# Optimization experiments

Measured on AMD Instinct MI355X. Metric: run time of the kernel, lower is better.

## Reference

```python
import jax, jax.numpy as jnp
import numpy as np

EPS = 1e-12


def setup_inputs() -> dict:
    key = jax.random.key(0)
    n, k, Eu, iterations = 200_000, 7, 1_600_000, 3
    k1, k2, k3 = jax.random.split(key, 3)
    # undirected edge list; each undirected edge yields two directed edges
    su = jax.random.randint(k1, (Eu,), 0, n, dtype=jnp.int32)
    du = jax.random.randint(k2, (Eu,), 0, n, dtype=jnp.int32)
    src = jnp.concatenate([su, du])                                   # [E]
    dst = jnp.concatenate([du, su])                                   # [E]
    rev = jnp.concatenate([jnp.arange(Eu, 2 * Eu, dtype=jnp.int32),
                           jnp.arange(Eu, dtype=jnp.int32)])          # [E]
    # node priors (rows sum to 1), mimicking the soft label priors
    prior = jax.random.uniform(k3, (n, k), minval=0.1, maxval=1.0)
    prior = prior / prior.sum(axis=1, keepdims=True)
    # label-to-label potential: log(beta) on the diagonal (beta = 3.0)
    W = jnp.log(3.0) * jnp.eye(k, dtype=jnp.float32)
    return {"prior": prior, "W": W, "src": src, "dst": dst,
            "rev": rev, "iterations": iterations}


def reference(prior, W, src, dst, rev, iterations):
    n, k = prior.shape
    E = src.shape[0]
    psi = jnp.exp(jnp.clip(W, -10.0, 10.0))                           # [k,k]
    msgs = jnp.full((E, k), 1.0 / k, dtype=prior.dtype)

    def step(msgs, _):
        # product of incoming messages per node, in log-space (msgs >= EPS)
        logm = jnp.log(msgs)                                          # [E,k]
        logP = jax.ops.segment_sum(logm, dst, num_segments=n)         # [n,k]
        # per directed edge (i -> j): remove reverse message j -> i
        prod_in_i = jnp.exp(logP[src] - logm[rev])                    # [E,k]
        b = jnp.maximum(prior[src] * prod_in_i, EPS)                  # [E,k]
        m_new = jnp.maximum(b @ psi, EPS)                             # [E,k]
        m_new = m_new / jnp.maximum(m_new.sum(-1, keepdims=True), EPS)
        return m_new, None

    msgs, _ = jax.lax.scan(step, msgs, None, length=int(iterations))

    # beliefs
    logP = jax.ops.segment_sum(jnp.log(msgs), dst, num_segments=n)    # [n,k]
    b = jnp.maximum(prior * jnp.exp(logP), EPS)
    return b / jnp.maximum(b.sum(-1, keepdims=True), EPS)
```

## Files before the change

### kernel.cpp

```cpp
#include <hip/hip_runtime.h>
#include <hip/hip_bf16.h>

#define K 7
#define EPSF 1e-12f
#define LOG_INV_K (-1.9459101090932196f)
#define LOG7 1.9459101090932196f
#define NEG_LOG_EPS 27.631021f
#define SBN 512
#define SBSH 9
#define NSBMAX 768
#define PB 256

#define QSB 409.59375f
#define QSO 2047.96875f
#define QIB (160.0f / 65535.0f)
#define QIO (32.0f / 65535.0f)

__device__ __forceinline__ float ldf(const void* p, size_t idx, int mode) {
    return mode ? ((const float*)p)[idx]
                : __bfloat162float(((const __hip_bfloat16*)p)[idx]);
}

__device__ __forceinline__ void load_psi(const void* W, float* psi, int mode) {
    if (threadIdx.x < K * K) {
        float w = ldf(W, threadIdx.x, mode);
        w = fminf(fmaxf(w, -10.f), 10.f);
        psi[threadIdx.x] = __expf(w);
    }
    __syncthreads();
}

__device__ __forceinline__ void bp_lin(const float* b, const float* psi, float* m) {
    float o[K], sum = 0.f;
#pragma unroll
    for (int j = 0; j < K; j++) {
        float acc = 0.f;
#pragma unroll
        for (int i = 0; i < K; i++) acc += b[i] * psi[i * K + j];
        o[j] = fmaxf(acc, EPSF);
        sum += o[j];
    }
    float inv = __fdividef(1.f, fmaxf(sum, EPSF));
#pragma unroll
    for (int j = 0; j < K; j++) m[j] = o[j] * inv;
}

__device__ __forceinline__ void acc_log_msg(const float* b, const float* psi, float* acc) {
    float m[K];
    bp_lin(b, psi, m);
#pragma unroll
    for (int j = 0; j < K; j++) acc[j] += __logf(m[j]);
}

__device__ __forceinline__ void ld8(const float* base, float* r) {
    const float4* p = (const float4*)base;
    float4 a = p[0], b = p[1];
    r[0]=a.x; r[1]=a.y; r[2]=a.z; r[3]=a.w; r[4]=b.x; r[5]=b.y; r[6]=b.z; r[7]=b.w;
}

__device__ __forceinline__ void dec_pd(uint4 w, float* p, int* degv, int* u1) {
    p[0] = __uint_as_float((w.x & 0xffffu) << 16);
    p[1] = __uint_as_float(w.x & 0xffff0000u);
    p[2] = __uint_as_float((w.y & 0xffffu) << 16);
    p[3] = __uint_as_float(w.y & 0xffff0000u);
    p[4] = __uint_as_float((w.z & 0xffffu) << 16);
    p[5] = __uint_as_float(w.z & 0xffff0000u);
    p[6] = __uint_as_float((w.w & 0xffffu) << 16);
    *degv = (int)((w.w >> 16) & 0x7fffu);
    *u1 = (int)(w.w >> 31);
}

__device__ __forceinline__ uint4 enc_log7(const float* le) {
    float mx = le[0];
#pragma unroll
    for (int i = 1; i < K; i++) mx = fmaxf(mx, le[i]);
    float nb = fminf(fmaxf(-mx, 0.f), 159.9f);
    unsigned qb = (unsigned)(nb * QSB + 0.5f);
    unsigned qo[K];
#pragma unroll
    for (int i = 0; i < K; i++)
        qo[i] = (unsigned)(fminf(mx - le[i], 31.98f) * QSO + 0.5f);
    uint4 r;
    r.x = qb | (qo[0] << 16);
    r.y = qo[1] | (qo[2] << 16);
    r.z = qo[3] | (qo[4] << 16);
    r.w = qo[5] | (qo[6] << 16);
    return r;
}

__device__ __forceinline__ void dec_exp7(uint4 w, float* e) {
    float base = (float)(w.x & 0xffffu) * QIB;
    float o[K];
    o[0] = (float)(w.x >> 16) * QIO;
    o[1] = (float)(w.y & 0xffffu) * QIO;
    o[2] = (float)(w.y >> 16) * QIO;
    o[3] = (float)(w.z & 0xffffu) * QIO;
    o[4] = (float)(w.z >> 16) * QIO;
    o[5] = (float)(w.w & 0xffffu) * QIO;
    o[6] = (float)(w.w >> 16) * QIO;
#pragma unroll
    for (int i = 0; i < K; i++) e[i] = __expf(-(base + o[i]));
}

__global__ void sniff8_kernel(const void* __restrict__ W, int* __restrict__ prm) {
    if (blockIdx.x != 0 || threadIdx.x != 0) return;
    const unsigned int* Wraw = (const unsigned int*)W;
    int mode = ((Wraw[0] >> 16) != 0u) ? 1 : 0;
    float diag0 = 0.f, offd0 = 0.f;
    int structured = 1;
    for (int i = 0; i < K; i++)
        for (int j = 0; j < K; j++) {
            float w = ldf(W, i * K + j, mode);
            w = fminf(fmaxf(w, -10.f), 10.f);
            float e = __expf(w);
            if (i == 0 && j == 0) diag0 = e;
            if (i == 0 && j == 1) offd0 = e;
            if (i == j) { if (i > 0 && e != diag0) structured = 0; }
            else       { if (!(i == 0 && j == 1) && e != offd0) structured = 0; }
        }
    if (!(offd0 >= 0.2f) || !(diag0 >= offd0)) structured = 0;
    prm[0] = mode | (structured << 1);
    ((float*)prm)[1] = offd0;
    ((float*)prm)[2] = diag0;
}

__global__ void hist6_kernel(const int* __restrict__ dst, int* __restrict__ hist,
                             int* __restrict__ btot, int E, int EPB, int NSB) {
    __shared__ int h[NSBMAX];
    for (int i = threadIdx.x; i < NSB; i += 256) h[i] = 0;
    __syncthreads();
    int blk = blockIdx.x;
    int e0 = blk * EPB, e1 = min(e0 + EPB, E);
    for (int e = e0 + (int)threadIdx.x; e < e1; e += 256)
        atomicAdd(&h[dst[e] >> SBSH], 1);
    __syncthreads();
    for (int i = threadIdx.x; i < NSB; i += 256) {
        int c = h[i];
        hist[i * PB + blk] = c;
        if (c) atomicAdd(&btot[i], c);
    }
}

__global__ void bscan6_kernel(const int* __restrict__ btot, int* __restrict__ boff, int NSB) {
    __shared__ int s[1024];
    int t = threadIdx.x;
    int x = (t < NSB) ? btot[t] : 0;
    s[t] = x;
    __syncthreads();
    for (int o = 1; o < 1024; o <<= 1) {
        int y = (t >= o) ? s[t - o] : 0;
        __syncthreads();
        s[t] += y;
        __syncthreads();
    }
    if (t < NSB) boff[t] = s[t] - x;
    if (t == NSB - 1) boff[NSB] = s[t];
}

__global__ void sscan6_kernel(const int* __restrict__ hist, const int* __restrict__ boff,
                              int* __restrict__ woff) {
    __shared__ int s[PB];
    int b = blockIdx.x, t = threadIdx.x;
    int x = hist[b * PB + t];
    s[t] = x;
    __syncthreads();
    for (int o = 1; o < PB; o <<= 1) {
        int y = (t >= o) ? s[t - o] : 0;
        __syncthreads();
        s[t] += y;
        __syncthreads();
    }
    woff[b * PB + t] = boff[b] + s[t] - x;
}

__global__ void part6_kernel(const int* __restrict__ src, const int* __restrict__ dst,
                             const int* __restrict__ woff, unsigned int* __restrict__ coarse,
                             int E, int EPB, int NSB) {
    __shared__ int cur[NSBMAX];
    int blk = blockIdx.x;
    for (int i = threadIdx.x; i < NSB; i += 256) cur[i] = woff[i * PB + blk];
    __syncthreads();
    int e0 = blk * EPB, e1 = min(e0 + EPB, E);
    for (int e = e0 + (int)threadIdx.x; e < e1; e += 256) {
        int d = dst[e];
        int b = d >> SBSH;
        unsigned int pk = (unsigned int)src[e] | ((unsigned int)(d & (SBN - 1)) << 18);
        int pos = atomicAdd(&cur[b], 1);
        coarse[pos] = pk;
    }
}

__global__ void cfill6_kernel(const unsigned int* __restrict__ coarse,
                              const int* __restrict__ boff,
                              int* __restrict__ cur, int* __restrict__ nbr, int n) {
    __shared__ int lcnt[SBN], lcur[SBN];
    int b = blockIdx.x, t = threadIdx.x;
    for (int i = t; i < SBN; i += 256) lcnt[i] = 0;
    __syncthreads();
    int s0 = boff[b], s1 = boff[b + 1];
    for (int i = s0 + t; i < s1; i += 256)
        atomicAdd(&lcnt[coarse[i] >> 18], 1);
    __syncthreads();
    if (t == 0) {
        int a = s0;
        for (int l = 0; l < SBN; l++) { lcur[l] = a; a += lcnt[l]; }
    }
    __syncthreads();
    int v0 = b << SBSH;
    for (int i = t; i < SBN; i += 256)
        if (v0 + i < n) cur[v0 + i] = lcur[i] + lcnt[i];
    __syncthreads();
    for (int i = s0 + t; i < s1; i += 256) {
        unsigned int w = coarse[i];
        int pos = atomicAdd(&lcur[w >> 18], 1);
        nbr[pos] = (int)(w & 0x3FFFFu);
    }
}

__global__ void pdbuild8_kernel(const void* __restrict__ prior, const int* __restrict__ cur,
                                const int* __restrict__ prm, uint4* __restrict__ PD,
                                unsigned int* __restrict__ UBM, int n) {
    int v = blockIdx.x * 256 + threadIdx.x;
    int mode = prm[0] & 1;
    int valid = (v < n);
    int degv = 0;
    unsigned int pb[K];
    float p[K];
#pragma unroll
    for (int i = 0; i < K; i++) { pb[i] = 0; p[i] = 0.f; }
    if (valid) {
        int start = v ? cur[v - 1] : 0;
        degv = cur[v] - start;
        if (mode == 0) {
            const unsigned short* pr = (const unsigned short*)prior;
#pragma unroll
            for (int i = 0; i < K; i++) {
                pb[i] = pr[(size_t)v * K + i];
                p[i] = __uint_as_float(pb[i] << 16);
            }
        } else {
            const float* pr = (const float*)prior;
#pragma unroll
            for (int i = 0; i < K; i++) {
                p[i] = pr[(size_t)v * K + i];
                __hip_bfloat16 h = __float2bfloat16(p[i]);
                pb[i] = *(unsigned short*)&h;
            }
        }
    }
    float es = __expf((float)(degv - 1) * LOG_INV_K);
    float mx = p[0];
#pragma unroll
    for (int i = 1; i < K; i++) mx = fmaxf(mx, p[i]);
    int u1 = (valid && (mx * es <= EPSF)) ? 1 : 0;
    unsigned long long mask = __ballot(u1);
    if ((threadIdx.x & 63) == 0) {
        int w0 = (blockIdx.x * 256 + ((int)threadIdx.x & ~63)) >> 5;
        UBM[w0] = (unsigned int)mask;
        UBM[w0 + 1] = (unsigned int)(mask >> 32);
    }
    if (!valid) return;
    int dcap = degv > 0x7fff ? 0x7fff : degv;
    uint4 w;
    w.x = pb[0] | (pb[1] << 16);
    w.y = pb[2] | (pb[3] << 16);
    w.z = pb[4] | (pb[5] << 16);
    w.w = pb[6] | (((unsigned int)dcap) << 16) | ((unsigned int)u1 << 31);
    PD[v] = w;
}

__global__ void n2v8_kernel(const int* __restrict__ cur, const int* __restrict__ nbr,
                            const uint4* __restrict__ PD, const unsigned int* __restrict__ UBM,
                            const void* __restrict__ W, const int* __restrict__ prm,
                            uint4* __restrict__ LP1, float* __restrict__ EP1f, int n) {
    __shared__ float psi[K * K];
    int pm = prm[0];
    int mode = pm & 1, strq = (pm >> 1) & 1;
    float offd = ((const float*)prm)[1], diag = ((const float*)prm)[2];
    load_psi(W, psi, mode);
    int t = blockIdx.x * blockDim.x + threadIdx.x;
    int v = t >> 1, h = t & 1;
    if (v >= n) return;
    int start = v ? cur[v - 1] : 0, end = cur[v];
    int degv = end - start;
    int mid = start + (degv >> 1);
    int lo = h ? mid : start, hi = h ? end : mid;
    float cb = diag - offd;
    float acc[K];
    int cn = 0;
    if (strq) {
#pragma unroll
        for (int i = 0; i < K; i++) acc[i] = 1.f;
        for (int e = lo; e < hi; e++) {
            int u = nbr[e];
            if ((UBM[u >> 5] >> (u & 31)) & 1u) continue;
            float p[K]; int degu, uu;
            dec_pd(PD[u], p, &degu, &uu);
            float es = __expf((float)(degu - 1) * LOG_INV_K);
            float b[K], S = 0.f;
#pragma unroll
            for (int i = 0; i < K; i++) { b[i] = fmaxf(p[i] * es, EPSF); S += b[i]; }
            float crS = __fdividef(cb, S);
#pragma unroll
            for (int i = 0; i < K; i++) acc[i] *= fmaf(crS, b[i], offd);
            cn++;
        }
#pragma unroll
        for (int i = 0; i < K; i++) acc[i] *= __shfl_xor(acc[i], 1, 64);
    } else {
#pragma unroll
        for (int i = 0; i < K; i++) acc[i] = 0.f;
        for (int e = lo; e < hi; e++) {
            int u = nbr[e];
            float p[K]; int degu, uu;
            dec_pd(PD[u], p, &degu, &uu);
            float es = __expf((float)(degu - 1) * LOG_INV_K);
            float b[K];
#pragma unroll
            for (int i = 0; i < K; i++) b[i] = fmaxf(p[i] * es, EPSF);
            acc_log_msg(b, psi, acc);
        }
#pragma unroll
        for (int i = 0; i < K; i++) acc[i] += __shfl_xor(acc[i], 1, 64);
    }
    cn += __shfl_xor(cn, 1, 64);
    if (h) return;
    float pv[K]; int dv, u1v;
    dec_pd(PD[v], pv, &dv, &u1v);
    float le[K];
    if (strq) {
        float corr = (float)cn * __logf(6.f * offd + diag) + (float)(degv - cn) * LOG7;
#pragma unroll
        for (int i = 0; i < K; i++) le[i] = __logf(pv[i] * acc[i]) - corr;
    } else {
#pragma unroll
        for (int i = 0; i < K; i++) le[i] = __logf(pv[i]) + acc[i];
    }
    LP1[v] = enc_log7(le);
    float4* q = (float4*)(EP1f + (size_t)v * 8);
    q[0] = make_float4(__expf(le[0]), __expf(le[1]), __expf(le[2]), __expf(le[3]));
    q[1] = make_float4(__expf(le[4]), __expf(le[5]), __expf(le[6]), 0.f);
}

__global__ void n3v8_kernel(const int* __restrict__ cur, const int* __restrict__ nbr,
                            const uint4* __restrict__ PD, const uint4* __restrict__ LP1,
                            const void* __restrict__ W, const int* __restrict__ prm,
                            uint4* __restrict__ Q2, int n) {
    __shared__ float psi[K * K];
    int pm = prm[0];
    int mode = pm & 1, strq = (pm >> 1) & 1;
    float offd = ((const float*)prm)[1], diag = ((const float*)prm)[2];
    load_psi(W, psi, mode);
    int t = blockIdx.x * blockDim.x + threadIdx.x;
    int v = t >> 1, h = t & 1;
    if (v >= n) return;
    int start = v ? cur[v - 1] : 0, end = cur[v];
    int degv = end - start;
    int mid = start + (degv >> 1);
    int lo = h ? mid : start, hi = h ? end : mid;
    float cb = diag - offd, norm = 6.f * offd + diag;
    uint4 pdv = PD[v];
    float pv[K]; int dv, u1v;
    dec_pd(pdv, pv, &dv, &u1v);
    float rm1v[K], mrv = 0.f;
    if (strq && u1v) {
#pragma unroll
        for (int i = 0; i < K; i++) rm1v[i] = 7.f;
        mrv = 7.f;
    } else {
        float es = __expf((float)(dv - 1) * LOG_INV_K);
        float b1[K], S1 = 0.f;
#pragma unroll
        for (int i = 0; i < K; i++) { b1[i] = fmaxf(pv[i] * es, EPSF); S1 += b1[i]; }
        if (strq) {
            float inv = __fdividef(1.f, S1 * norm);
#pragma unroll
            for (int i = 0; i < K; i++) {
                float m1 = (offd * S1 + cb * b1[i]) * inv;
                rm1v[i] = __fdividef(1.f, m1);
                mrv = fmaxf(mrv, rm1v[i]);
            }
        } else {
            float m1[K];
            bp_lin(b1, psi, m1);
#pragma unroll
            for (int i = 0; i < K; i++) rm1v[i] = __fdividef(1.f, m1[i]);
        }
    }
    float acc[K];
    int cn = 0;
    if (strq) {
        int tqv = (int)((__logf(mrv) + NEG_LOG_EPS) * QSB) + 1;
#pragma unroll
        for (int i = 0; i < K; i++) acc[i] = 1.f;
        for (int e = lo; e < hi; e++) {
            int u = nbr[e];
            uint4 q = LP1[u];
            if ((int)(q.x & 0xffffu) >= tqv) continue;
            float eu[K];
            dec_exp7(q, eu);
            float b[K], S = 0.f;
#pragma unroll
            for (int i = 0; i < K; i++) { b[i] = fmaxf(eu[i] * rm1v[i], EPSF); S += b[i]; }
            float crS = __fdividef(cb, S);
#pragma unroll
            for (int i = 0; i < K; i++) acc[i] *= fmaf(crS, b[i], offd);
            cn++;
        }
#pragma unroll
        for (int i = 0; i < K; i++) acc[i] *= __shfl_xor(acc[i], 1, 64);
    } else {
#pragma unroll
        for (int i = 0; i < K; i++) acc[i] = 0.f;
        for (int e = lo; e < hi; e++) {
            int u = nbr[e];
            float eu[K];
            dec_exp7(LP1[u], eu);
            float b[K];
#pragma unroll
            for (int i = 0; i < K; i++) b[i] = fmaxf(eu[i] * rm1v[i], EPSF);
            acc_log_msg(b, psi, acc);
        }
#pragma unroll
        for (int i = 0; i < K; i++) acc[i] += __shfl_xor(acc[i], 1, 64);
    }
    cn += __shfl_xor(cn, 1, 64);
    if (h) return;
    float le2[K];
    if (strq) {
        float corr = (float)cn * __logf(norm) + (float)(degv - cn) * LOG7;
#pragma unroll
        for (int i = 0; i < K; i++) le2[i] = __logf(pv[i] * acc[i]) - corr;
    } else {
#pragma unroll
        for (int i = 0; i < K; i++) le2[i] = __logf(pv[i]) + acc[i];
    }
    Q2[v] = enc_log7(le2);
}

__global__ void n4v8_kernel(const int* __restrict__ cur, const int* __restrict__ nbr,
                            const uint4* __restrict__ PD, const uint4* __restrict__ Q2,
                            const float* __restrict__ EP1f, const void* __restrict__ prior,
                            const void* __restrict__ W, const int* __restrict__ prm,
                            void* __restrict__ out, int n) {
    __shared__ float psi[K * K];
    int pm = prm[0];
    int mode = pm & 1, strq = (pm >> 1) & 1;
    float offd = ((const float*)prm)[1], diag = ((const float*)prm)[2];
    load_psi(W, psi, mode);
    int t = blockIdx.x * blockDim.x + threadIdx.x;
    int v = t >> 1, h = t & 1;
    if (v >= n) return;
    int start = v ? cur[v - 1] : 0, end = cur[v];
    int degv = end - start;
    int mid = start + (degv >> 1);
    int lo = h ? mid : start, hi = h ? end : mid;
    float cb = diag - offd, norm = 6.f * offd + diag;
    float e1v[8];
    ld8(EP1f + (size_t)v * 8, e1v);
    float acc[K];
    int cn = 0;
    if (strq) {
        float mx1 = e1v[0];
#pragma unroll
        for (int i = 1; i < K; i++) mx1 = fmaxf(mx1, e1v[i]);
        float F = __fdividef(norm, offd) * 1.01f;
        int m2u = (F * mx1 <= EPSF);
        int tq2c = (int)((LOG7 + NEG_LOG_EPS) * QSB) + 1;
#pragma unroll
        for (int i = 0; i < K; i++) acc[i] = 1.f;
        if (m2u) {
            for (int e = lo; e < hi; e++) {
                int u = nbr[e];
                uint4 q = Q2[u];
                if ((int)(q.x & 0xffffu) >= tq2c) continue;
                float e2[K];
                dec_exp7(q, e2);
                float b3[K], S = 0.f;
#pragma unroll
                for (int i = 0; i < K; i++) { b3[i] = fmaxf(7.f * e2[i], EPSF); S += b3[i]; }
                float crS = __fdividef(cb, S);
#pragma unroll
                for (int i = 0; i < K; i++) acc[i] *= fmaf(crS, b3[i], offd);
                cn++;
            }
        } else {
            for (int e = lo; e < hi; e++) {
                int u = nbr[e];
                uint4 q = Q2[u];
                uint4 pdu = PD[u];
                float pu[K]; int degu, u1u;
                dec_pd(pdu, pu, &degu, &u1u);
                float rm1u[K];
                if (u1u) {
#pragma unroll
                    for (int i = 0; i < K; i++) rm1u[i] = 7.f;
                } else {
                    float es = __expf((float)(degu - 1) * LOG_INV_K);
                    float b1[K], S1 = 0.f;
#pragma unroll
                    for (int i = 0; i < K; i++) { b1[i] = fmaxf(pu[i] * es, EPSF); S1 += b1[i]; }
                    float inv = __fdividef(1.f, S1 * norm);
#pragma unroll
                    for (int i = 0; i < K; i++)
                        rm1u[i] = __fdividef(1.f, (offd * S1 + cb * b1[i]) * inv);
                }
                float b2[K], S2 = 0.f;
#pragma unroll
                for (int i = 0; i < K; i++) { b2[i] = fmaxf(e1v[i] * rm1u[i], EPSF); S2 += b2[i]; }
                float inv2 = __fdividef(1.f, S2 * norm);
                float e2[K];
                dec_exp7(q, e2);
                float b3[K], S3 = 0.f;
#pragma unroll
                for (int i = 0; i < K; i++) {
                    float m2 = (offd * S2 + cb * b2[i]) * inv2;
                    b3[i] = fmaxf(__fdividef(e2[i], m2), EPSF);
                    S3 += b3[i];
                }
                float crS3 = __fdividef(cb, S3);
#pragma unroll
                for (int i = 0; i < K; i++) acc[i] *= fmaf(crS3, b3[i], offd);
                cn++;
            }
        }
#pragma unroll
        for (int i = 0; i < K; i++) acc[i] *= __shfl_xor(acc[i], 1, 64);
    } else {
#pragma unroll
        for (int i = 0; i < K; i++) acc[i] = 0.f;
        for (int e = lo; e < hi; e++) {
            int u = nbr[e];
            uint4 q = Q2[u];
            uint4 pdu = PD[u];
            float pu[K]; int degu, u1u;
            dec_pd(pdu, pu, &degu, &u1u);
            float es = __expf((float)(degu - 1) * LOG_INV_K);
            float b1[K], m1u[K];
#pragma unroll
            for (int i = 0; i < K; i++) b1[i] = fmaxf(pu[i] * es, EPSF);
            bp_lin(b1, psi, m1u);
            float b2[K], m2[K];
#pragma unroll
            for (int i = 0; i < K; i++) b2[i] = fmaxf(__fdividef(e1v[i], m1u[i]), EPSF);
            bp_lin(b2, psi, m2);
            float e2[K];
            dec_exp7(q, e2);
            float b3[K];
#pragma unroll
            for (int i = 0; i < K; i++) b3[i] = fmaxf(__fdividef(e2[i], m2[i]), EPSF);
            acc_log_msg(b3, psi, acc);
        }
#pragma unroll
        for (int i = 0; i < K; i++) acc[i] += __shfl_xor(acc[i], 1, 64);
    }
    cn += __shfl_xor(cn, 1, 64);
    if (h) return;
    float bb[K], sum = 0.f;
    if (strq) {
        float corr = (float)cn * __logf(norm) + (float)(degv - cn) * LOG7;
#pragma unroll
        for (int i = 0; i < K; i++) {
            float p = ldf(prior, (size_t)v * K + i, mode);
            bb[i] = fmaxf(__expf(__logf(p * acc[i]) - corr), EPSF);
            sum += bb[i];
        }
    } else {
#pragma unroll
        for (int i = 0; i < K; i++) {
            float p = ldf(prior, (size_t)v * K + i, mode);
            bb[i] = fmaxf(p * __expf(acc[i]), EPSF);
            sum += bb[i];
        }
    }
    float inv = __fdividef(1.f, fmaxf(sum, EPSF));
#pragma unroll
    for (int i = 0; i < K; i++) {
        float val = bb[i] * inv;
        if (mode) ((float*)out)[(size_t)v * K + i] = val;
        else ((__hip_bfloat16*)out)[(size_t)v * K + i] = __float2bfloat16(val);
    }
}

__device__ __forceinline__ void bp_msg(const float* b, const float* psi, float* lm) {
    float m[K];
    bp_lin(b, psi, m);
#pragma unroll
    for (int j = 0; j < K; j++) lm[j] = __logf(m[j]);
}
__device__ __forceinline__ void msg1(const void* prior, int node, int degv, int mode,
                                     const float* psi, float* lm) {
    float es = __expf((float)(degv - 1) * LOG_INV_K);
    float b[K];
#pragma unroll
    for (int i = 0; i < K; i++)
        b[i] = fmaxf(ldf(prior, (size_t)node * K + i, mode) * es, EPSF);
    bp_msg(b, psi, lm);
}
__device__ __forceinline__ void msgF(const void* prior, int node,
                                     const float* __restrict__ logP,
                                     const float* lmrev, int mode,
                                     const float* psi, float* lm) {
    float b[K];
#pragma unroll
    for (int i = 0; i < K; i++)
        b[i] = fmaxf(ldf(prior, (size_t)node * K + i, mode) *
                     __expf(logP[(size_t)node * K + i] - lmrev[i]), EPSF);
    bp_msg(b, psi, lm);
}
__global__ void deg_kernel(const int* __restrict__ su, const int* __restrict__ du,
                           int* __restrict__ deg, int Eu) {
    int u = blockIdx.x * blockDim.x + threadIdx.x;
    if (u >= Eu) return;
    atomicAdd(&deg[su[u]], 1);
    atomicAdd(&deg[du[u]], 1);
}
__global__ void pass1_kernel(const int* __restrict__ su, const int* __restrict__ du,
                             const int* __restrict__ deg, const void* __restrict__ prior,
                             const void* __restrict__ W, const int* __restrict__ prm,
                             float* __restrict__ logP1, int Eu) {
    __shared__ float psi[K * K];
    int mode = prm[0] & 1;
    load_psi(W, psi, mode);
    int u = blockIdx.x * blockDim.x + threadIdx.x;
    if (u >= Eu) return;
    int s = su[u], d = du[u];
    float lm[K];
    msg1(prior, s, deg[s], mode, psi, lm);
#pragma unroll
    for (int j = 0; j < K; j++) atomicAdd(&logP1[(size_t)d * K + j], lm[j]);
    msg1(prior, d, deg[d], mode, psi, lm);
#pragma unroll
    for (int j = 0; j < K; j++) atomicAdd(&logP1[(size_t)s * K + j], lm[j]);
}
__global__ void pass2_kernel(const int* __restrict__ su, const int* __restrict__ du,
                             const int* __restrict__ deg, const void* __restrict__ prior,
                             const void* __restrict__ W, const int* __restrict__ prm,
                             const float* __restrict__ logP1, float* __restrict__ logP2, int Eu) {
    __shared__ float psi[K * K];
    int mode = prm[0] & 1;
    load_psi(W, psi, mode);
    int u = blockIdx.x * blockDim.x + threadIdx.x;
    if (u >= Eu) return;
    int s = su[u], d = du[u];
    float lm1sd[K], lm1ds[K], lm[K];
    msg1(prior, s, deg[s], mode, psi, lm1sd);
    msg1(prior, d, deg[d], mode, psi, lm1ds);
    msgF(prior, s, logP1, lm1ds, mode, psi, lm);
#pragma unroll
    for (int j = 0; j < K; j++) atomicAdd(&logP2[(size_t)d * K + j], lm[j]);
    msgF(prior, d, logP1, lm1sd, mode, psi, lm);
#pragma unroll
    for (int j = 0; j < K; j++) atomicAdd(&logP2[(size_t)s * K + j], lm[j]);
}
__global__ void pass3_kernel(const int* __restrict__ su, const int* __restrict__ du,
                             const int* __restrict__ deg, const void* __restrict__ prior,
                             const void* __restrict__ W, const int* __restrict__ prm,
                             const float* __restrict__ logP1, const float* __restrict__ logP2,
                             float* __restrict__ logP3, int Eu) {
    __shared__ float psi[K * K];
    int mode = prm[0] & 1;
    load_psi(W, psi, mode);
    int u = blockIdx.x * blockDim.x + threadIdx.x;
    if (u >= Eu) return;
    int s = su[u], d = du[u];
    float lm1sd[K], lm1ds[K], lm2sd[K], lm2ds[K], lm[K];
    msg1(prior, s, deg[s], mode, psi, lm1sd);
    msg1(prior, d, deg[d], mode, psi, lm1ds);
    msgF(prior, s, logP1, lm1ds, mode, psi, lm2sd);
    msgF(prior, d, logP1, lm1sd, mode, psi, lm2ds);
    msgF(prior, s, logP2, lm2ds, mode, psi, lm);
#pragma unroll
    for (int j = 0; j < K; j++) atomicAdd(&logP3[(size_t)d * K + j], lm[j]);
    msgF(prior, d, logP2, lm2sd, mode, psi, lm);
#pragma unroll
    for (int j = 0; j < K; j++) atomicAdd(&logP3[(size_t)s * K + j], lm[j]);
}
__global__ void belief_kernel(const float* __restrict__ logP3, const void* __restrict__ prior,
                              const int* __restrict__ prm, void* __restrict__ out, int n) {
    int v = blockIdx.x * blockDim.x + threadIdx.x;
    if (v >= n) return;
    int mode = prm[0] & 1;
    float b[K], sum = 0.f;
#pragma unroll
    for (int j = 0; j < K; j++) {
        b[j] = fmaxf(ldf(prior, (size_t)v * K + j, mode) * __expf(logP3[(size_t)v * K + j]), EPSF);
        sum += b[j];
    }
    float inv = __fdividef(1.f, fmaxf(sum, EPSF));
#pragma unroll
    for (int j = 0; j < K; j++) {
        float val = b[j] * inv;
        if (mode) ((float*)out)[(size_t)v * K + j] = val;
        else ((__hip_bfloat16*)out)[(size_t)v * K + j] = __float2bfloat16(val);
    }
}

extern "C" void kernel_launch(void* const* d_in, const int* in_sizes, int n_in,
                              void* d_out, int out_size, void* d_ws, size_t ws_size,
                              hipStream_t stream) {
    const void* prior = d_in[0];
    const void* W     = d_in[1];
    const int* src = (const int*)d_in[2];
    const int* dst = (const int*)d_in[3];

    int n  = in_sizes[0] / K;
    int E  = in_sizes[2];
    int Eu = E / 2;

    const int B = 256;
    int gn  = (n + B - 1) / B;
    int gn2 = (2 * n + B - 1) / B;
    int ge  = (Eu + B - 1) / B;

    char* ws = (char*)d_ws;
    size_t off = 0;
    auto alloc = [&](size_t bytes) { size_t o = off; off = (off + bytes + 127) & ~(size_t)127; return o; };

    size_t xsz = (size_t)E * 4;
    if ((size_t)n * 48 > xsz) xsz = (size_t)n * 48;
    size_t o_nbr  = alloc((size_t)E * 4);
    size_t o_X    = alloc(xsz);
    size_t o_EP1f = alloc((size_t)n * 32);
    size_t o_cur  = alloc((size_t)n * 4);
    size_t o_hist = alloc((size_t)NSBMAX * PB * 4);
    size_t o_woff = alloc((size_t)NSBMAX * PB * 4);
    size_t o_boff = alloc((size_t)(NSBMAX + 1) * 4);
    size_t o_btot = alloc((size_t)NSBMAX * 4);
    size_t o_ubm  = alloc((size_t)gn * 8 * 4 + 64);
    size_t o_prm  = alloc(64);
    size_t need_v8 = off;

    int NSB = (n + SBN - 1) >> SBSH;
    int EPB = (E + PB - 1) / PB;

    bool v8_ok = (ws_size >= need_v8) && (n <= (1 << 18)) && (NSB <= NSBMAX) && (NSB >= 1);

    if (v8_ok) {
        int*   nbr    = (int*)(ws + o_nbr);
        unsigned int* coarse = (unsigned int*)(ws + o_X);
        uint4* PD     = (uint4*)(ws + o_X);
        uint4* LP1    = (uint4*)(ws + o_X + (size_t)n * 16);
        uint4* Q2     = (uint4*)(ws + o_X + (size_t)n * 32);
        float* EP1f   = (float*)(ws + o_EP1f);
        int*   cur    = (int*)(ws + o_cur);
        int*   hist   = (int*)(ws + o_hist);
        int*   woff   = (int*)(ws + o_woff);
        int*   boff   = (int*)(ws + o_boff);
        int*   btot   = (int*)(ws + o_btot);
        unsigned int* UBM = (unsigned int*)(ws + o_ubm);
        int*   prm    = (int*)(ws + o_prm);

        sniff8_kernel<<<1, 64, 0, stream>>>(W, prm);
        hipMemsetAsync(btot, 0, (size_t)NSB * 4, stream);
        hist6_kernel<<<PB, B, 0, stream>>>(dst, hist, btot, E, EPB, NSB);
        bscan6_kernel<<<1, 1024, 0, stream>>>(btot, boff, NSB);
        sscan6_kernel<<<NSB, PB, 0, stream>>>(hist, boff, woff);
        part6_kernel<<<PB, B, 0, stream>>>(src, dst, woff, coarse, E, EPB, NSB);
        cfill6_kernel<<<NSB, B, 0, stream>>>(coarse, boff, cur, nbr, n);
        pdbuild8_kernel<<<gn, B, 0, stream>>>(prior, cur, prm, PD, UBM, n);
        n2v8_kernel<<<gn2, B, 0, stream>>>(cur, nbr, PD, UBM, W, prm, LP1, EP1f, n);
        n3v8_kernel<<<gn2, B, 0, stream>>>(cur, nbr, PD, LP1, W, prm, Q2, n);
        n4v8_kernel<<<gn2, B, 0, stream>>>(cur, nbr, PD, Q2, EP1f, prior, W, prm, d_out, n);
        return;
    }

    {
        float* logP1 = (float*)d_ws;
        float* logP2 = logP1 + (size_t)n * K;
        float* logP3 = logP2 + (size_t)n * K;
        int*   deg   = (int*)(logP3 + (size_t)n * K);
        int*   prm   = deg + n;
        sniff8_kernel<<<1, 64, 0, stream>>>(W, prm - 0);
        hipMemsetAsync(d_ws, 0, ((size_t)3 * n * K + n) * sizeof(float), stream);
        deg_kernel<<<ge, B, 0, stream>>>(src, dst, deg, Eu);
        pass1_kernel<<<ge, B, 0, stream>>>(src, dst, deg, prior, W, prm, logP1, Eu);
        pass2_kernel<<<ge, B, 0, stream>>>(src, dst, deg, prior, W, prm, logP1, logP2, Eu);
        pass3_kernel<<<ge, B, 0, stream>>>(src, dst, deg, prior, W, prm, logP1, logP2, logP3, Eu);
        belief_kernel<<<gn, B, 0, stream>>>(logP3, prior, prm, d_out, n);
    }
}
```

Before: 327.3 us.

## Fuse PD build into CSR fill, use 4 threads per node, add skip filter

Builds the packed prior/degree records (PD) inside the CSR fill kernel, which removes one launch and one read of the offsets array. The separate underflow bitmask goes away, and the skip test now reads the flag bit from the PD record that is loaded anyway. Each node's neighbour list is split across four lanes instead of two, combined with two xor-shuffle rounds, to raise parallelism on the irregular gathers. A new threshold test on Q2 in the final pass skips neighbours whose contribution is judged negligible, which could shift accuracy if the threshold is not conservative.

```diff
diff --git a/kernel.cpp b/kernel.cpp
--- a/kernel.cpp
+++ b/kernel.cpp
@@ -190,11 +190,14 @@
     }
 }
 
-__global__ void cfill6_kernel(const unsigned int* __restrict__ coarse,
+__global__ void cfill9_kernel(const unsigned int* __restrict__ coarse,
                               const int* __restrict__ boff,
-                              int* __restrict__ cur, int* __restrict__ nbr, int n) {
+                              const void* __restrict__ prior, const int* __restrict__ prm,
+                              int* __restrict__ cur, int* __restrict__ nbr,
+                              uint4* __restrict__ PD, int n) {
     __shared__ int lcnt[SBN], lcur[SBN];
     int b = blockIdx.x, t = threadIdx.x;
+    int mode = prm[0] & 1;
     for (int i = t; i < SBN; i += 256) lcnt[i] = 0;
     __syncthreads();
     int s0 = boff[b], s1 = boff[b + 1];
@@ -207,8 +210,42 @@
     }
     __syncthreads();
     int v0 = b << SBSH;
-    for (int i = t; i < SBN; i += 256)
-        if (v0 + i < n) cur[v0 + i] = lcur[i] + lcnt[i];
+    for (int i = t; i < SBN; i += 256) {
+        int v = v0 + i;
+        if (v >= n) continue;
+        int degv = lcnt[i];
+        cur[v] = lcur[i] + degv;
+        unsigned int pb[K];
+        float p[K];
+        if (mode == 0) {
+            const unsigned short* pr = (const unsigned short*)prior;
+#pragma unroll
+            for (int j = 0; j < K; j++) {
+                pb[j] = pr[(size_t)v * K + j];
+                p[j] = __uint_as_float(pb[j] << 16);
+            }
+        } else {
+            const float* pr = (const float*)prior;
+#pragma unroll
+            for (int j = 0; j < K; j++) {
+                p[j] = pr[(size_t)v * K + j];
+                __hip_bfloat16 hh = __float2bfloat16(p[j]);
+                pb[j] = *(unsigned short*)&hh;
+            }
+        }
+        float es = __expf((float)(degv - 1) * LOG_INV_K);
+        float mx = p[0];
+#pragma unroll
+        for (int j = 1; j < K; j++) mx = fmaxf(mx, p[j]);
+        unsigned int u1 = (mx * es <= EPSF) ? 1u : 0u;
+        int dcap = degv > 0x7fff ? 0x7fff : degv;
+        uint4 w;
+        w.x = pb[0] | (pb[1] << 16);
+        w.y = pb[2] | (pb[3] << 16);
+        w.z = pb[4] | (pb[5] << 16);
+        w.w = pb[6] | (((unsigned int)dcap) << 16) | (u1 << 31);
+        PD[v] = w;
+    }
     __syncthreads();
     for (int i = s0 + t; i < s1; i += 256) {
         unsigned int w = coarse[i];
@@ -217,74 +254,21 @@
     }
 }
 
-__global__ void pdbuild8_kernel(const void* __restrict__ prior, const int* __restrict__ cur,
-                                const int* __restrict__ prm, uint4* __restrict__ PD,
-                                unsigned int* __restrict__ UBM, int n) {
-    int v = blockIdx.x * 256 + threadIdx.x;
-    int mode = prm[0] & 1;
-    int valid = (v < n);
-    int degv = 0;
-    unsigned int pb[K];
-    float p[K];
-#pragma unroll
-    for (int i = 0; i < K; i++) { pb[i] = 0; p[i] = 0.f; }
-    if (valid) {
-        int start = v ? cur[v - 1] : 0;
-        degv = cur[v] - start;
-        if (mode == 0) {
-            const unsigned short* pr = (const unsigned short*)prior;
-#pragma unroll
-            for (int i = 0; i < K; i++) {
-                pb[i] = pr[(size_t)v * K + i];
-                p[i] = __uint_as_float(pb[i] << 16);
-            }
-        } else {
-            const float* pr = (const float*)prior;
-#pragma unroll
-            for (int i = 0; i < K; i++) {
-                p[i] = pr[(size_t)v * K + i];
-                __hip_bfloat16 h = __float2bfloat16(p[i]);
-                pb[i] = *(unsigned short*)&h;
-            }
-        }
-    }
-    float es = __expf((float)(degv - 1) * LOG_INV_K);
-    float mx = p[0];
-#pragma unroll
-    for (int i = 1; i < K; i++) mx = fmaxf(mx, p[i]);
-    int u1 = (valid && (mx * es <= EPSF)) ? 1 : 0;
-    unsigned long long mask = __ballot(u1);
-    if ((threadIdx.x & 63) == 0) {
-        int w0 = (blockIdx.x * 256 + ((int)threadIdx.x & ~63)) >> 5;
-        UBM[w0] = (unsigned int)mask;
-        UBM[w0 + 1] = (unsigned int)(mask >> 32);
-    }
-    if (!valid) return;
-    int dcap = degv > 0x7fff ? 0x7fff : degv;
-    uint4 w;
-    w.x = pb[0] | (pb[1] << 16);
-    w.y = pb[2] | (pb[3] << 16);
-    w.z = pb[4] | (pb[5] << 16);
-    w.w = pb[6] | (((unsigned int)dcap) << 16) | ((unsigned int)u1 << 31);
-    PD[v] = w;
-}
-
-__global__ void n2v8_kernel(const int* __restrict__ cur, const int* __restrict__ nbr,
-                            const uint4* __restrict__ PD, const unsigned int* __restrict__ UBM,
-                            const void* __restrict__ W, const int* __restrict__ prm,
-                            uint4* __restrict__ LP1, float* __restrict__ EP1f, int n) {
+__global__ void n2v9_kernel(const int* __restrict__ cur, const int* __restrict__ nbr,
+                            const uint4* __restrict__ PD, const void* __restrict__ W,
+                            const int* __restrict__ prm, uint4* __restrict__ LP1,
+                            float* __restrict__ EP1f, int n) {
     __shared__ float psi[K * K];
     int pm = prm[0];
     int mode = pm & 1, strq = (pm >> 1) & 1;
     float offd = ((const float*)prm)[1], diag = ((const float*)prm)[2];
     load_psi(W, psi, mode);
     int t = blockIdx.x * blockDim.x + threadIdx.x;
-    int v = t >> 1, h = t & 1;
+    int v = t >> 2, qi = t & 3;
     if (v >= n) return;
     int start = v ? cur[v - 1] : 0, end = cur[v];
-    int degv = end - start;
-    int mid = start + (degv >> 1);
-    int lo = h ? mid : start, hi = h ? end : mid;
+    int len = end - start;
+    int lo = start + ((len * qi) >> 2), hi = start + ((len * (qi + 1)) >> 2);
     float cb = diag - offd;
     float acc[K];
     int cn = 0;
@@ -293,9 +277,10 @@
         for (int i = 0; i < K; i++) acc[i] = 1.f;
         for (int e = lo; e < hi; e++) {
             int u = nbr[e];
-            if ((UBM[u >> 5] >> (u & 31)) & 1u) continue;
+            uint4 w = PD[u];
+            if (w.w >> 31) continue;
             float p[K]; int degu, uu;
-            dec_pd(PD[u], p, &degu, &uu);
+            dec_pd(w, p, &degu, &uu);
             float es = __expf((float)(degu - 1) * LOG_INV_K);
             float b[K], S = 0.f;
 #pragma unroll
@@ -306,7 +291,10 @@
             cn++;
         }
 #pragma unroll
-        for (int i = 0; i < K; i++) acc[i] *= __shfl_xor(acc[i], 1, 64);
+        for (int i = 0; i < K; i++) {
+            acc[i] *= __shfl_xor(acc[i], 1, 64);
+            acc[i] *= __shfl_xor(acc[i], 2, 64);
+        }
     } else {
 #pragma unroll
         for (int i = 0; i < K; i++) acc[i] = 0.f;
@@ -321,15 +309,19 @@
             acc_log_msg(b, psi, acc);
         }
 #pragma unroll
-        for (int i = 0; i < K; i++) acc[i] += __shfl_xor(acc[i], 1, 64);
+        for (int i = 0; i < K; i++) {
+            acc[i] += __shfl_xor(acc[i], 1, 64);
+            acc[i] += __shfl_xor(acc[i], 2, 64);
+        }
     }
     cn += __shfl_xor(cn, 1, 64);
-    if (h) return;
+    cn += __shfl_xor(cn, 2, 64);
+    if (qi) return;
     float pv[K]; int dv, u1v;
     dec_pd(PD[v], pv, &dv, &u1v);
     float le[K];
     if (strq) {
-        float corr = (float)cn * __logf(6.f * offd + diag) + (float)(degv - cn) * LOG7;
+        float corr = (float)cn * __logf(6.f * offd + diag) + (float)(len - cn) * LOG7;
 #pragma unroll
         for (int i = 0; i < K; i++) le[i] = __logf(pv[i] * acc[i]) - corr;
     } else {
@@ -342,7 +334,7 @@
     q[1] = make_float4(__expf(le[4]), __expf(le[5]), __expf(le[6]), 0.f);
 }
 
-__global__ void n3v8_kernel(const int* __restrict__ cur, const int* __restrict__ nbr,
+__global__ void n3v9_kernel(const int* __restrict__ cur, const int* __restrict__ nbr,
                             const uint4* __restrict__ PD, const uint4* __restrict__ LP1,
                             const void* __restrict__ W, const int* __restrict__ prm,
                             uint4* __restrict__ Q2, int n) {
@@ -352,12 +344,11 @@
     float offd = ((const float*)prm)[1], diag = ((const float*)prm)[2];
     load_psi(W, psi, mode);
     int t = blockIdx.x * blockDim.x + threadIdx.x;
-    int v = t >> 1, h = t & 1;
+    int v = t >> 2, qi = t & 3;
     if (v >= n) return;
     int start = v ? cur[v - 1] : 0, end = cur[v];
-    int degv = end - start;
-    int mid = start + (degv >> 1);
-    int lo = h ? mid : start, hi = h ? end : mid;
+    int len = end - start;
+    int lo = start + ((len * qi) >> 2), hi = start + ((len * (qi + 1)) >> 2);
     float cb = diag - offd, norm = 6.f * offd + diag;
     uint4 pdv = PD[v];
     float pv[K]; int dv, u1v;
@@ -408,7 +399,10 @@
             cn++;
         }
 #pragma unroll
-        for (int i = 0; i < K; i++) acc[i] *= __shfl_xor(acc[i], 1, 64);
+        for (int i = 0; i < K; i++) {
+            acc[i] *= __shfl_xor(acc[i], 1, 64);
+            acc[i] *= __shfl_xor(acc[i], 2, 64);
+        }
     } else {
 #pragma unroll
         for (int i = 0; i < K; i++) acc[i] = 0.f;
@@ -422,13 +416,17 @@
             acc_log_msg(b, psi, acc);
         }
 #pragma unroll
-        for (int i = 0; i < K; i++) acc[i] += __shfl_xor(acc[i], 1, 64);
+        for (int i = 0; i < K; i++) {
+            acc[i] += __shfl_xor(acc[i], 1, 64);
+            acc[i] += __shfl_xor(acc[i], 2, 64);
+        }
     }
     cn += __shfl_xor(cn, 1, 64);
-    if (h) return;
+    cn += __shfl_xor(cn, 2, 64);
+    if (qi) return;
     float le2[K];
     if (strq) {
-        float corr = (float)cn * __logf(norm) + (float)(degv - cn) * LOG7;
+        float corr = (float)cn * __logf(norm) + (float)(len - cn) * LOG7;
 #pragma unroll
         for (int i = 0; i < K; i++) le2[i] = __logf(pv[i] * acc[i]) - corr;
     } else {
@@ -438,7 +436,7 @@
     Q2[v] = enc_log7(le2);
 }
 
-__global__ void n4v8_kernel(const int* __restrict__ cur, const int* __restrict__ nbr,
+__global__ void n4v9_kernel(const int* __restrict__ cur, const int* __restrict__ nbr,
                             const uint4* __restrict__ PD, const uint4* __restrict__ Q2,
                             const float* __restrict__ EP1f, const void* __restrict__ prior,
                             const void* __restrict__ W, const int* __restrict__ prm,
@@ -449,12 +447,11 @@
     float offd = ((const float*)prm)[1], diag = ((const float*)prm)[2];
     load_psi(W, psi, mode);
     int t = blockIdx.x * blockDim.x + threadIdx.x;
-    int v = t >> 1, h = t & 1;
+    int v = t >> 2, qi = t & 3;
     if (v >= n) return;
     int start = v ? cur[v - 1] : 0, end = cur[v];
-    int degv = end - start;
-    int mid = start + (degv >> 1);
-    int lo = h ? mid : start, hi = h ? end : mid;
+    int len = end - start;
+    int lo = start + ((len * qi) >> 2), hi = start + ((len * (qi + 1)) >> 2);
     float cb = diag - offd, norm = 6.f * offd + diag;
     float e1v[8];
     ld8(EP1f + (size_t)v * 8, e1v);
@@ -467,6 +464,7 @@
         float F = __fdividef(norm, offd) * 1.01f;
         int m2u = (F * mx1 <= EPSF);
         int tq2c = (int)((LOG7 + NEG_LOG_EPS) * QSB) + 1;
+        int tq3  = (int)((__logf(F) + NEG_LOG_EPS) * QSB) + 1;
 #pragma unroll
         for (int i = 0; i < K; i++) acc[i] = 1.f;
         if (m2u) {
@@ -488,6 +486,7 @@
             for (int e = lo; e < hi; e++) {
                 int u = nbr[e];
                 uint4 q = Q2[u];
+                if ((int)(q.x & 0xffffu) >= tq3) continue;
                 uint4 pdu = PD[u];
                 float pu[K]; int degu, u1u;
                 dec_pd(pdu, pu, &degu, &u1u);
@@ -525,7 +524,10 @@
             }
         }
 #pragma unroll
-        for (int i = 0; i < K; i++) acc[i] *= __shfl_xor(acc[i], 1, 64);
+        for (int i = 0; i < K; i++) {
+            acc[i] *= __shfl_xor(acc[i], 1, 64);
+            acc[i] *= __shfl_xor(acc[i], 2, 64);
+        }
     } else {
 #pragma unroll
         for (int i = 0; i < K; i++) acc[i] = 0.f;
@@ -552,13 +554,17 @@
             acc_log_msg(b3, psi, acc);
         }
 #pragma unroll
-        for (int i = 0; i < K; i++) acc[i] += __shfl_xor(acc[i], 1, 64);
+        for (int i = 0; i < K; i++) {
+            acc[i] += __shfl_xor(acc[i], 1, 64);
+            acc[i] += __shfl_xor(acc[i], 2, 64);
+        }
     }
     cn += __shfl_xor(cn, 1, 64);
-    if (h) return;
+    cn += __shfl_xor(cn, 2, 64);
+    if (qi) return;
     float bb[K], sum = 0.f;
     if (strq) {
-        float corr = (float)cn * __logf(norm) + (float)(degv - cn) * LOG7;
+        float corr = (float)cn * __logf(norm) + (float)(len - cn) * LOG7;
 #pragma unroll
         for (int i = 0; i < K; i++) {
             float p = ldf(prior, (size_t)v * K + i, mode);
@@ -710,45 +716,44 @@
 
     const int B = 256;
     int gn  = (n + B - 1) / B;
-    int gn2 = (2 * n + B - 1) / B;
+    int gn4 = (4 * n + B - 1) / B;
     int ge  = (Eu + B - 1) / B;
+
+    int NSB = (n + SBN - 1) >> SBSH;
+    int EPB = (E + PB - 1) / PB;
 
     char* ws = (char*)d_ws;
     size_t off = 0;
     auto alloc = [&](size_t bytes) { size_t o = off; off = (off + bytes + 127) & ~(size_t)127; return o; };
 
     size_t xsz = (size_t)E * 4;
-    if ((size_t)n * 48 > xsz) xsz = (size_t)n * 48;
+    if ((size_t)n * 32 > xsz) xsz = (size_t)n * 32;
     size_t o_nbr  = alloc((size_t)E * 4);
     size_t o_X    = alloc(xsz);
+    size_t o_PD   = alloc((size_t)n * 16);
     size_t o_EP1f = alloc((size_t)n * 32);
     size_t o_cur  = alloc((size_t)n * 4);
-    size_t o_hist = alloc((size_t)NSBMAX * PB * 4);
-    size_t o_woff = alloc((size_t)NSBMAX * PB * 4);
-    size_t o_boff = alloc((size_t)(NSBMAX + 1) * 4);
-    size_t o_btot = alloc((size_t)NSBMAX * 4);
-    size_t o_ubm  = alloc((size_t)gn * 8 * 4 + 64);
+    size_t o_hist = alloc((size_t)NSB * PB * 4);
+    size_t o_woff = alloc((size_t)NSB * PB * 4);
+    size_t o_boff = alloc((size_t)(NSB + 1) * 4);
+    size_t o_btot = alloc((size_t)NSB * 4);
     size_t o_prm  = alloc(64);
-    size_t need_v8 = off;
-
-    int NSB = (n + SBN - 1) >> SBSH;
-    int EPB = (E + PB - 1) / PB;
-
-    bool v8_ok = (ws_size >= need_v8) && (n <= (1 << 18)) && (NSB <= NSBMAX) && (NSB >= 1);
-
-    if (v8_ok) {
+    size_t need_v9 = off;
+
+    bool v9_ok = (ws_size >= need_v9) && (n <= (1 << 18)) && (NSB <= NSBMAX) && (NSB >= 1);
+
+    if (v9_ok) {
         int*   nbr    = (int*)(ws + o_nbr);
         unsigned int* coarse = (unsigned int*)(ws + o_X);
-        uint4* PD     = (uint4*)(ws + o_X);
-        uint4* LP1    = (uint4*)(ws + o_X + (size_t)n * 16);
-        uint4* Q2     = (uint4*)(ws + o_X + (size_t)n * 32);
+        uint4* LP1    = (uint4*)(ws + o_X);
+        uint4* Q2     = (uint4*)(ws + o_X + (size_t)n * 16);
+        uint4* PD     = (uint4*)(ws + o_PD);
         float* EP1f   = (float*)(ws + o_EP1f);
         int*   cur    = (int*)(ws + o_cur);
         int*   hist   = (int*)(ws + o_hist);
         int*   woff   = (int*)(ws + o_woff);
         int*   boff   = (int*)(ws + o_boff);
         int*   btot   = (int*)(ws + o_btot);
-        unsigned int* UBM = (unsigned int*)(ws + o_ubm);
         int*   prm    = (int*)(ws + o_prm);
 
         sniff8_kernel<<<1, 64, 0, stream>>>(W, prm);
@@ -757,11 +762,10 @@
         bscan6_kernel<<<1, 1024, 0, stream>>>(btot, boff, NSB);
         sscan6_kernel<<<NSB, PB, 0, stream>>>(hist, boff, woff);
         part6_kernel<<<PB, B, 0, stream>>>(src, dst, woff, coarse, E, EPB, NSB);
-        cfill6_kernel<<<NSB, B, 0, stream>>>(coarse, boff, cur, nbr, n);
-        pdbuild8_kernel<<<gn, B, 0, stream>>>(prior, cur, prm, PD, UBM, n);
-        n2v8_kernel<<<gn2, B, 0, stream>>>(cur, nbr, PD, UBM, W, prm, LP1, EP1f, n);
-        n3v8_kernel<<<gn2, B, 0, stream>>>(cur, nbr, PD, LP1, W, prm, Q2, n);
-        n4v8_kernel<<<gn2, B, 0, stream>>>(cur, nbr, PD, Q2, EP1f, prior, W, prm, d_out, n);
+        cfill9_kernel<<<NSB, B, 0, stream>>>(coarse, boff, prior, prm, cur, nbr, PD, n);
+        n2v9_kernel<<<gn4, B, 0, stream>>>(cur, nbr, PD, W, prm, LP1, EP1f, n);
+        n3v9_kernel<<<gn4, B, 0, stream>>>(cur, nbr, PD, LP1, W, prm, Q2, n);
+        n4v9_kernel<<<gn4, B, 0, stream>>>(cur, nbr, PD, Q2, EP1f, prior, W, prm, d_out, n);
         return;
     }
 
@@ -771,7 +775,7 @@
         float* logP3 = logP2 + (size_t)n * K;
         int*   deg   = (int*)(logP3 + (size_t)n * K);
         int*   prm   = deg + n;
-        sniff8_kernel<<<1, 64, 0, stream>>>(W, prm - 0);
+        sniff8_kernel<<<1, 64, 0, stream>>>(W, prm);
         hipMemsetAsync(d_ws, 0, ((size_t)3 * n * K + n) * sizeof(float), stream);
         deg_kernel<<<ge, B, 0, stream>>>(src, dst, deg, Eu);
         pass1_kernel<<<ge, B, 0, stream>>>(src, dst, deg, prior, W, prm, logP1, Eu);
```

Measured after the change: 325.0 us. No clear change (-0.7%).
